# Performance work log

Hardware: AMD Instinct MI355X
Metric: run time of the kernel (lower is better)

## Reference

```python
import jax, jax.numpy as jnp
import numpy as np

B, L, D, H = 2, 2048, 768, 12
DH = D // H          # 64
DFF = 4 * D          # 3072
ALPHA = 0.25         # lorentz_alpha
BLEND = 0.5          # blend for FFN and MinkowskiLayerNorm (set via set_blend)
EPS = 1e-5
SCALE = float(np.sqrt(DH))


def setup_inputs() -> dict:
    key = jax.random.key(0)
    ks = jax.random.split(key, 14)
    w = lambda k, shape: jax.random.normal(k, shape, jnp.float32) * 0.02
    causal = jnp.tril(jnp.ones((L, L), bool))
    attention_mask = jnp.where(causal, 0.0, -1e9).astype(jnp.float32)[None, None]
    return {
        'x': jax.random.normal(ks[0], (B, L, D), jnp.float32),
        'attention_mask': attention_mask,
        'timelike_mask': jax.random.bernoulli(ks[1], 0.25, (D,)),
        'Wq': w(ks[2], (D, D)), 'Wk': w(ks[3], (D, D)),
        'Wv': w(ks[4], (D, D)), 'Wo': w(ks[5], (D, D)),
        'w1': w(ks[6], (DFF, D)), 'w2': w(ks[7], (D, DFF)),
        'w1_t': w(ks[8], (DFF // 2, D)), 'w2_t': w(ks[9], (D, DFF // 2)),
        'w1_s': w(ks[10], (DFF // 2, D)), 'w2_s': w(ks[11], (D, DFF // 2)),
        'n1_w': jnp.ones(D, jnp.float32), 'n1_b': jnp.zeros(D, jnp.float32),
        'n2_w': jnp.ones(D, jnp.float32), 'n2_b': jnp.zeros(D, jnp.float32),
    }


def _mink_norm(x, m, w, b):
    # Minkowski LayerNorm blended with standard LN (m: float timelike mask)
    mean = x.mean(-1, keepdims=True)
    xc = x - mean
    var = (xc * xc).mean(-1, keepdims=True)
    x_std = xc / jnp.sqrt(var + EPS)
    sq = xc * xc
    eta = (sq * (1.0 - m)).sum(-1, keepdims=True) - (sq * m).sum(-1, keepdims=True)
    x_eta = xc / jnp.sqrt(jnp.abs(eta) + EPS)
    xn = (1.0 - BLEND) * x_std + BLEND * x_eta
    return w * xn + b


def _attn(x, attention_mask, m, Wq, Wk, Wv, Wo):
    # (B,L,D) -> (B,H,L,DH)
    split = lambda t: t.reshape(B, L, H, DH).transpose(0, 2, 1, 3)
    Q = split(x @ Wq.T)
    K = split(x @ Wk.T)
    V = split(x @ Wv.T)
    scores = jnp.einsum('bhqd,bhkd->bhqk', Q, K) / SCALE
    # Minkowski timelike correction: per-head diagonal mask on Q
    m2 = m.reshape(H, DH)[None, :, None, :]          # (1,H,1,DH)
    Q_t = Q * m2
    q_norm = jnp.linalg.norm(Q, axis=-1, keepdims=True)
    qt_norm = jnp.linalg.norm(Q_t, axis=-1, keepdims=True)
    sf = jnp.where(qt_norm > 1e-6, q_norm / jnp.maximum(qt_norm, 1e-8), 0.0)
    time_inner = jnp.einsum('bhqd,bhkd->bhqk', Q_t * sf, K) / SCALE
    scores = scores - 2.0 * ALPHA * time_inner
    scores = scores + attention_mask
    aw = jax.nn.softmax(scores, axis=-1)
    out = jnp.einsum('bhqk,bhkd->bhqd', aw, V)
    out = out.transpose(0, 2, 1, 3).reshape(B, L, D)
    return out @ Wo.T


def _ffn(x, m, w1, w2, w1_t, w2_t, w1_s, w2_s):
    std_out = jax.nn.gelu(x @ w1.T, approximate=False) @ w2.T
    h_t = jax.nn.silu((x * m) @ w1_t.T) @ w2_t.T
    h_s = jax.nn.gelu((x * (1.0 - m)) @ w1_s.T, approximate=False) @ w2_s.T
    return (1.0 - BLEND) * std_out + BLEND * (h_t + h_s)


def reference(x, attention_mask, timelike_mask, Wq, Wk, Wv, Wo,
              w1, w2, w1_t, w2_t, w1_s, w2_s, n1_w, n1_b, n2_w, n2_b):
    m = timelike_mask.astype(jnp.float32)
    ao = _attn(_mink_norm(x, m, n1_w, n1_b), attention_mask, m, Wq, Wk, Wv, Wo)
    x = x + ao
    x = x + _ffn(_mink_norm(x, m, n2_w, n2_b), m, w1, w2, w1_t, w2_t, w1_s, w2_s)
    return x
```

## Files before the change

### kernel.cpp

```cpp
#include <hip/hip_runtime.h>


typedef unsigned short u16;
typedef __bf16 bfrag __attribute__((ext_vector_type(8)));
typedef float f32x4 __attribute__((ext_vector_type(4)));

#define MFMA(a, b, c) __builtin_amdgcn_mfma_f32_16x16x32_bf16(a, b, c, 0, 0, 0)
#define NEG_BIG (-30000.0f)
#define ASYNC16(g, l)                                                        \
  __builtin_amdgcn_global_load_lds(                                          \
      (const __attribute__((address_space(1))) unsigned int*)(g),            \
      (__attribute__((address_space(3))) unsigned int*)(l), 16, 0, 0)

__device__ __forceinline__ float bf2f(u16 u) {
  unsigned int v = ((unsigned int)u) << 16;
  float f; __builtin_memcpy(&f, &v, 4); return f;
}
__device__ __forceinline__ u16 f2bf(float f) {
  unsigned int v; __builtin_memcpy(&v, &f, 4);
  v += 0x7fffu + ((v >> 16) & 1u);
  return (u16)(v >> 16);
}
__device__ __forceinline__ bfrag ldfrag(const u16* p) {
  bfrag v; __builtin_memcpy(&v, p, 16); return v;
}

__device__ __forceinline__ int xcd_work_id() {
  const int nx = gridDim.x, ny = gridDim.y;
  const int nwg = nx * ny * gridDim.z;
  const int orig = blockIdx.x + nx * (blockIdx.y + ny * blockIdx.z);
  if (nwg & 7) return orig;
  return (orig & 7) * (nwg >> 3) + (orig >> 3);
}

__global__ __launch_bounds__(256) void mask_conv_k(const void* __restrict__ mask,
                                                   float* __restrict__ mfl) {
  __shared__ int msh;
  if (threadIdx.x == 0) msh = 0;
  __syncthreads();
  const unsigned int* w = (const unsigned int*)mask;
  if (threadIdx.x < 192) {
    const unsigned int v = w[threadIdx.x];
    if ((v & 0xFFFFu) == 0x3F80u) atomicOr(&msh, 4);
    else if (v == 0x3F800000u) atomicOr(&msh, 2);
    else if (v >= 2u) atomicOr(&msh, 1);
  }
  __syncthreads();
  const int m = msh;
  const int mode = (m & 4) ? 3 : (m & 2) ? 2 : (m & 1) ? 1 : 0;
  for (int i = threadIdx.x; i < 768; i += 256) {
    int b;
    if (mode == 3) b = ((const u16*)mask)[i] != 0;
    else if (mode == 2) b = ((const float*)mask)[i] != 0.0f;
    else if (mode == 1) b = ((const unsigned char*)mask)[i] != 0;
    else b = ((const int*)mask)[i] != 0;
    mfl[i] = (float)b;
  }
}

struct Segs {
  const void* src[14];
  int off[14];
  int n[14];
  int mmode[14];
};

__global__ __launch_bounds__(256) void convert_k(Segs segs, u16* __restrict__ dstb,
                                                 const float* __restrict__ mfl) {
  const int seg = blockIdx.y;
  const int n = segs.n[seg];
  const int mm = segs.mmode[seg];
  u16* dst = dstb + segs.off[seg];
  const float* src = (const float*)segs.src[seg];
  for (int i = (blockIdx.x * 256 + threadIdx.x) * 4; i < n; i += gridDim.x * 1024) {
    float4 v;
    __builtin_memcpy(&v, src + i, 16);
    if (mm) {
      const int k = i % 768;
      float m0 = mfl[k], m1 = mfl[k + 1], m2 = mfl[k + 2], m3 = mfl[k + 3];
      if (mm == 2) { m0 = 1.f - m0; m1 = 1.f - m1; m2 = 1.f - m2; m3 = 1.f - m3; }
      v.x *= m0; v.y *= m1; v.z *= m2; v.w *= m3;
    }
    dst[i] = f2bf(v.x); dst[i + 1] = f2bf(v.y);
    dst[i + 2] = f2bf(v.z); dst[i + 3] = f2bf(v.w);
  }
}

__global__ __launch_bounds__(256) void mink_norm_k(
    const float* __restrict__ X, const float* __restrict__ mf,
    const u16* __restrict__ w, const u16* __restrict__ bias,
    u16* __restrict__ Y, float* __restrict__ Xcopy) {
  __shared__ float red[8];
  const int row = blockIdx.x, tid = threadIdx.x;
  const int wid = tid >> 6, lane = tid & 63;
  const size_t roff = (size_t)row * 768;

  float xv[3], mv[3];
  int idx[3];
#pragma unroll
  for (int i = 0; i < 3; i++) {
    idx[i] = tid + i * 256;
    xv[i] = X[roff + idx[i]];
    mv[i] = mf[idx[i]];
  }
  if (Xcopy) {
#pragma unroll
    for (int i = 0; i < 3; i++) Xcopy[roff + idx[i]] = xv[i];
  }
  float s = xv[0] + xv[1] + xv[2];
#pragma unroll
  for (int o = 32; o >= 1; o >>= 1) s += __shfl_xor(s, o, 64);
  if (lane == 0) red[wid] = s;
  __syncthreads();
  const float mean = (red[0] + red[1] + red[2] + red[3]) * (1.0f / 768.0f);
  __syncthreads();

  float xc[3], ss = 0.0f, sm = 0.0f;
#pragma unroll
  for (int i = 0; i < 3; i++) {
    xc[i] = xv[i] - mean;
    ss += xc[i] * xc[i];
    sm += xc[i] * xc[i] * mv[i];
  }
#pragma unroll
  for (int o = 32; o >= 1; o >>= 1) {
    ss += __shfl_xor(ss, o, 64);
    sm += __shfl_xor(sm, o, 64);
  }
  if (lane == 0) { red[wid] = ss; red[4 + wid] = sm; }
  __syncthreads();
  const float sumsq = red[0] + red[1] + red[2] + red[3];
  const float summ = red[4] + red[5] + red[6] + red[7];
  const float var = sumsq * (1.0f / 768.0f);
  const float eta = sumsq - 2.0f * summ;
  const float rs = 1.0f / sqrtf(var + 1e-5f);
  const float re = 1.0f / sqrtf(fabsf(eta) + 1e-5f);

#pragma unroll
  for (int i = 0; i < 3; i++) {
    const float xn = xc[i] * 0.5f * (rs + re);
    Y[roff + idx[i]] = f2bf(bf2f(w[idx[i]]) * xn + bf2f(bias[idx[i]]));
  }
}

__global__ __launch_bounds__(256) void qcorr_k(u16* __restrict__ Q,
                                               const float* __restrict__ mf) {
  const int idx = blockIdx.x * 4 + (threadIdx.x >> 6);
  const int t = threadIdx.x & 63;
  const int h = idx % 12;
  const int bl = idx / 12;
  const size_t off = (size_t)bl * 768 + h * 64 + t;
  const float q = bf2f(Q[off]);
  const float m = mf[h * 64 + t];
  float q2 = q * q, qm2 = q * q * m;
#pragma unroll
  for (int o = 32; o >= 1; o >>= 1) {
    q2 += __shfl_xor(q2, o, 64);
    qm2 += __shfl_xor(qm2, o, 64);
  }
  const float qn = sqrtf(q2), qtn = sqrtf(qm2);
  const float sf = (qtn > 1e-6f) ? qn / fmaxf(qtn, 1e-8f) : 0.0f;
  Q[off] = f2bf(q * (1.0f - 0.5f * sf * m) * 0.125f);
}

__device__ __forceinline__ void gemm128_loop(
    const u16* __restrict__ Ab, const u16* __restrict__ Wb2,
    int K, int lda, int ldb, u16 (*As)[32], u16 (*Bs)[32], f32x4 acc[4][4]) {
  const int tid = threadIdx.x;
  const int wid = tid >> 6, lane = tid & 63;
  const int lr = lane & 15, lq = lane >> 4;
  const int srow = wid * 32 + (lane >> 2);
  const int scol = (lane & 3) * 8;
  const u16* ga0 = Ab + (size_t)srow * lda + scol;
  const u16* ga1 = Ab + (size_t)(srow + 16) * lda + scol;
  const u16* gb0 = Wb2 + (size_t)srow * ldb + scol;
  const u16* gb1 = Wb2 + (size_t)(srow + 16) * ldb + scol;
  const int wr = (wid >> 1) * 64, wc = (wid & 1) * 64;
  const int nt = K >> 5;

#define STAGE16(dbuf, k0)                                                    \
  {                                                                          \
    u16* _a0 = &As[(dbuf) * 128 + wid * 32][0];                              \
    u16* _a1 = &As[(dbuf) * 128 + wid * 32 + 16][0];                         \
    u16* _b0 = &Bs[(dbuf) * 128 + wid * 32][0];                              \
    u16* _b1 = &Bs[(dbuf) * 128 + wid * 32 + 16][0];                         \
    ASYNC16(ga0 + (k0), _a0);                                                \
    ASYNC16(ga1 + (k0), _a1);                                                \
    ASYNC16(gb0 + (k0), _b0);                                                \
    ASYNC16(gb1 + (k0), _b1);                                                \
  }

  STAGE16(0, 0);
  for (int t = 0; t < nt; ++t) {
    const int cur = t & 1;
    if (t + 1 < nt) {
      STAGE16(cur ^ 1, (t + 1) << 5);
      __builtin_amdgcn_sched_barrier(0);
      asm volatile("s_waitcnt vmcnt(4)" ::: "memory");
    } else {
      asm volatile("s_waitcnt vmcnt(0)" ::: "memory");
    }
    __builtin_amdgcn_s_barrier();
    __builtin_amdgcn_sched_barrier(0);
    bfrag af[4], bf4[4];
#pragma unroll
    for (int i = 0; i < 4; i++)
      af[i] = ldfrag(&As[cur * 128 + wr + i * 16 + lr][lq * 8]);
#pragma unroll
    for (int j = 0; j < 4; j++)
      bf4[j] = ldfrag(&Bs[cur * 128 + wc + j * 16 + lr][lq * 8]);
#pragma unroll
    for (int i = 0; i < 4; i++)
#pragma unroll
      for (int j = 0; j < 4; j++)
        acc[i][j] = MFMA(af[i], bf4[j], acc[i][j]);
    asm volatile("s_waitcnt lgkmcnt(0)" ::: "memory");
    __builtin_amdgcn_sched_barrier(0);
    __builtin_amdgcn_s_barrier();
  }
#undef STAGE16
}

__device__ __forceinline__ void gemm128x64_loop(
    const u16* __restrict__ Ab, const u16* __restrict__ Wb2,
    int K, int lda, int ldb, u16 (*As)[32], u16 (*Bs)[32], f32x4 acc[4][2]) {
  const int tid = threadIdx.x;
  const int wid = tid >> 6, lane = tid & 63;
  const int lr = lane & 15, lq = lane >> 4;
  const int srowA = wid * 32 + (lane >> 2);
  const int srowB = wid * 16 + (lane >> 2);
  const int scol = (lane & 3) * 8;
  const u16* ga0 = Ab + (size_t)srowA * lda + scol;
  const u16* ga1 = Ab + (size_t)(srowA + 16) * lda + scol;
  const u16* gb0 = Wb2 + (size_t)srowB * ldb + scol;
  const int wr = (wid >> 1) * 64, wc = (wid & 1) * 32;
  const int nt = K >> 5;

#define STAGE64(dbuf, k0)                                                    \
  {                                                                          \
    u16* _a0 = &As[(dbuf) * 128 + wid * 32][0];                              \
    u16* _a1 = &As[(dbuf) * 128 + wid * 32 + 16][0];                         \
    u16* _b0 = &Bs[(dbuf) * 64 + wid * 16][0];                               \
    ASYNC16(ga0 + (k0), _a0);                                                \
    ASYNC16(ga1 + (k0), _a1);                                                \
    ASYNC16(gb0 + (k0), _b0);                                                \
  }

  STAGE64(0, 0);
  for (int t = 0; t < nt; ++t) {
    const int cur = t & 1;
    if (t + 1 < nt) {
      STAGE64(cur ^ 1, (t + 1) << 5);
      __builtin_amdgcn_sched_barrier(0);
      asm volatile("s_waitcnt vmcnt(3)" ::: "memory");
    } else {
      asm volatile("s_waitcnt vmcnt(0)" ::: "memory");
    }
    __builtin_amdgcn_s_barrier();
    __builtin_amdgcn_sched_barrier(0);
    bfrag af[4], bf2[2];
#pragma unroll
    for (int i = 0; i < 4; i++)
      af[i] = ldfrag(&As[cur * 128 + wr + i * 16 + lr][lq * 8]);
#pragma unroll
    for (int j = 0; j < 2; j++)
      bf2[j] = ldfrag(&Bs[cur * 64 + wc + j * 16 + lr][lq * 8]);
#pragma unroll
    for (int i = 0; i < 4; i++)
#pragma unroll
      for (int j = 0; j < 2; j++)
        acc[i][j] = MFMA(af[i], bf2[j], acc[i][j]);
    asm volatile("s_waitcnt lgkmcnt(0)" ::: "memory");
    __builtin_amdgcn_sched_barrier(0);
    __builtin_amdgcn_s_barrier();
  }
#undef STAGE64
}

struct GSeg { const u16* W; u16* C; int ldc; int nblk; int epi; };
struct GArgs { GSeg s[3]; };

__global__ __launch_bounds__(256) void gemm128_fused(
    const u16* __restrict__ A, int lda, int K, GArgs args) {
  __shared__ __align__(16) u16 As[256][32];
  __shared__ __align__(16) u16 Bs[256][32];
  const int w = xcd_work_id();
  int cb = w % gridDim.x, seg = 0;
  const int by = w / gridDim.x;
  while (cb >= args.s[seg].nblk) { cb -= args.s[seg].nblk; seg++; }
  const GSeg g = args.s[seg];
  const int rowb = by * 128, colb = cb * 128;
  f32x4 acc[4][4] = {};
  gemm128_loop(A + (size_t)rowb * lda, g.W + (size_t)colb * K, K, lda, K,
               As, Bs, acc);

  const int lane = threadIdx.x & 63, wid = threadIdx.x >> 6;
  const int lr = lane & 15, lq = lane >> 4;
  const int wr = (wid >> 1) * 64, wc = (wid & 1) * 64;
#pragma unroll
  for (int i = 0; i < 4; i++)
#pragma unroll
    for (int j = 0; j < 4; j++)
#pragma unroll
      for (int r = 0; r < 4; r++) {
        const int row = rowb + wr + i * 16 + lq * 4 + r;
        const int col = colb + wc + j * 16 + lr;
        float v = acc[i][j][r];
        if (g.epi == 2) v = 0.5f * v * (1.0f + erff(v * 0.70710678118654752f));
        else if (g.epi == 3) v = v / (1.0f + __expf(-v));
        g.C[(size_t)row * g.ldc + col] = f2bf(v);
      }
}

__global__ __launch_bounds__(256) void gemm128_wo_splitk(
    const u16* __restrict__ A, const u16* __restrict__ W,
    float* __restrict__ Out) {
  __shared__ __align__(16) u16 As[256][32];
  __shared__ __align__(16) u16 Bs[256][32];
  const int w = xcd_work_id();
  const int bx = w % gridDim.x;
  const int by = (w / gridDim.x) % gridDim.y;
  const int z = w / (gridDim.x * gridDim.y);
  const int rowb = by * 128, colb = bx * 128;
  f32x4 acc[4][4] = {};
  gemm128_loop(A + (size_t)rowb * 768 + z * 384,
               W + (size_t)colb * 768 + z * 384, 384, 768, 768, As, Bs, acc);

  const int lane = threadIdx.x & 63, wid = threadIdx.x >> 6;
  const int lr = lane & 15, lq = lane >> 4;
  const int wr = (wid >> 1) * 64, wc = (wid & 1) * 64;
#pragma unroll
  for (int i = 0; i < 4; i++)
#pragma unroll
    for (int j = 0; j < 4; j++)
#pragma unroll
      for (int r = 0; r < 4; r++) {
        const int row = rowb + wr + i * 16 + lq * 4 + r;
        const int col = colb + wc + j * 16 + lr;
        atomicAdd(&Out[(size_t)row * 768 + col], acc[i][j][r]);
      }
}

__global__ __launch_bounds__(256) void ffn2_splitk64(
    const u16* __restrict__ H1, const u16* __restrict__ Ht,
    const u16* __restrict__ Hs, const u16* __restrict__ W2,
    const u16* __restrict__ W2t, const u16* __restrict__ W2s,
    float* __restrict__ Out) {
  __shared__ __align__(16) u16 As[256][32];
  __shared__ __align__(16) u16 Bs[128][32];
  const int w = xcd_work_id();
  const int bx = w % gridDim.x;
  const int by = (w / gridDim.x) % gridDim.y;
  const int z = w / (gridDim.x * gridDim.y);
  const int rowb = by * 128, colb = bx * 64;
  f32x4 acc[4][2] = {};
  if (z == 0)
    gemm128x64_loop(H1 + (size_t)rowb * 3072, W2 + (size_t)colb * 3072,
                    1536, 3072, 3072, As, Bs, acc);
  else if (z == 1)
    gemm128x64_loop(H1 + (size_t)rowb * 3072 + 1536,
                    W2 + (size_t)colb * 3072 + 1536,
                    1536, 3072, 3072, As, Bs, acc);
  else if (z == 2)
    gemm128x64_loop(Ht + (size_t)rowb * 1536, W2t + (size_t)colb * 1536,
                    1536, 1536, 1536, As, Bs, acc);
  else
    gemm128x64_loop(Hs + (size_t)rowb * 1536, W2s + (size_t)colb * 1536,
                    1536, 1536, 1536, As, Bs, acc);

  const int lane = threadIdx.x & 63, wid = threadIdx.x >> 6;
  const int lr = lane & 15, lq = lane >> 4;
  const int wr = (wid >> 1) * 64, wc = (wid & 1) * 32;
#pragma unroll
  for (int i = 0; i < 4; i++)
#pragma unroll
    for (int j = 0; j < 2; j++)
#pragma unroll
      for (int r = 0; r < 4; r++) {
        const int row = rowb + wr + i * 16 + lq * 4 + r;
        const int col = colb + wc + j * 16 + lr;
        atomicAdd(&Out[(size_t)row * 768 + col], 0.5f * acc[i][j][r]);
      }
}

__global__ __launch_bounds__(256) void flash_attn_k(
    const u16* __restrict__ Qc, const u16* __restrict__ Kb,
    const u16* __restrict__ Vb, u16* __restrict__ O,
    float* __restrict__ Pn, float* __restrict__ Ph) {
  __shared__ __align__(16) u16 Ks[64][40];
  __shared__ __align__(16) u16 Vt[64][72];
  __shared__ __align__(16) u16 Ps[4][16][72];
  const int tid = threadIdx.x, wid = tid >> 6, lane = tid & 63;
  const int lr = lane & 15, lq = lane >> 4;

  int bx = blockIdx.x, qt = 0, c = 0;
  for (int q = 31; q >= 0; --q) {
    const int nc = (q < 8) ? 1 : (q / 8 + 1);
    if (bx < nc) { qt = q; c = bx; break; }
    bx -= nc;
  }
  const int nt = qt + 1;
  const int t0 = c * 8;
  const int t1 = (t0 + 8 < nt) ? t0 + 8 : nt;

  const int qb = qt * 64;
  const int bh = blockIdx.y;
  const int b = bh / 12, h = bh % 12;
  const int q0 = qb + wid * 16;
  const size_t base = (size_t)b * 2048 * 768 + h * 64;

  bfrag aq[2];
  aq[0] = ldfrag(Qc + base + (size_t)(q0 + lr) * 768 + lq * 8);
  aq[1] = ldfrag(Qc + base + (size_t)(q0 + lr) * 768 + 32 + lq * 8);

  f32x4 o[4] = {};
  float mrow[4] = {NEG_BIG, NEG_BIG, NEG_BIG, NEG_BIG};
  float lrow[4] = {0.0f, 0.0f, 0.0f, 0.0f};

  const int krow = tid >> 3;
  const int kcol = (tid & 7) * 8;
  const int vkey = tid & 31;
  const int vdg = tid >> 5;

  const u16* kp = Kb + base + (size_t)(t0 * 64 + krow) * 768 + kcol;
  const u16* vp = Vb + base + (size_t)(t0 * 64 + vkey) * 768 + vdg * 8;

  uint4 kv0, kv1, vv0, vv1;
  __builtin_memcpy(&kv0, kp, 16);
  __builtin_memcpy(&kv1, kp + (size_t)32 * 768, 16);
  __builtin_memcpy(&vv0, vp, 16);
  __builtin_memcpy(&vv1, vp + (size_t)32 * 768, 16);

  for (int kt = t0; kt < t1; kt++) {
    __syncthreads();
    __builtin_memcpy(&Ks[krow][kcol], &kv0, 16);
    __builtin_memcpy(&Ks[krow + 32][kcol], &kv1, 16);
    {
      union { uint4 u; u16 s[8]; } a, b2;
      a.u = vv0; b2.u = vv1;
#pragma unroll
      for (int j = 0; j < 8; j++) {
        Vt[vdg * 8 + j][vkey] = a.s[j];
        Vt[vdg * 8 + j][vkey + 32] = b2.s[j];
      }
    }
    __syncthreads();
    if (kt + 1 < t1) {
      const size_t koff = (size_t)(kt + 1 - t0) * 64 * 768;
      __builtin_memcpy(&kv0, kp + koff, 16);
      __builtin_memcpy(&kv1, kp + koff + (size_t)32 * 768, 16);
      __builtin_memcpy(&vv0, vp + koff, 16);
      __builtin_memcpy(&vv1, vp + koff + (size_t)32 * 768, 16);
    }

    const int kbk = kt * 64;
    {
      f32x4 s4[4] = {};
#pragma unroll
      for (int kg = 0; kg < 2; kg++) {
#pragma unroll
        for (int cc = 0; cc < 4; cc++) {
          bfrag bk = ldfrag(&Ks[cc * 16 + lr][kg * 32 + lq * 8]);
          s4[cc] = MFMA(aq[kg], bk, s4[cc]);
        }
      }
#pragma unroll
      for (int r = 0; r < 4; r++) {
        const int q = q0 + lq * 4 + r;
        float v[4];
        float mx = NEG_BIG;
#pragma unroll
        for (int cc = 0; cc < 4; cc++) {
          v[cc] = (kbk + cc * 16 + lr > q) ? NEG_BIG : s4[cc][r];
          mx = fmaxf(mx, v[cc]);
        }
#pragma unroll
        for (int off = 8; off >= 1; off >>= 1)
          mx = fmaxf(mx, __shfl_xor(mx, off, 16));
        const float mn = fmaxf(mrow[r], mx);
        const float alpha = __expf(mrow[r] - mn);
        float sm = 0.0f;
        float p[4];
#pragma unroll
        for (int cc = 0; cc < 4; cc++) {
          p[cc] = __expf(v[cc] - mn);
          sm += p[cc];
        }
#pragma unroll
        for (int off = 8; off >= 1; off >>= 1) sm += __shfl_xor(sm, off, 16);
        lrow[r] = lrow[r] * alpha + sm;
        mrow[r] = mn;
#pragma unroll
        for (int dt = 0; dt < 4; dt++) o[dt][r] *= alpha;
#pragma unroll
        for (int cc = 0; cc < 4; cc++)
          Ps[wid][lq * 4 + r][cc * 16 + lr] = f2bf(p[cc]);
      }
      __threadfence_block();
      bfrag pf0 = ldfrag(&Ps[wid][lr][lq * 8]);
      bfrag pf1 = ldfrag(&Ps[wid][lr][32 + lq * 8]);
#pragma unroll
      for (int dt = 0; dt < 4; dt++) {
        bfrag v0 = ldfrag(&Vt[dt * 16 + lr][lq * 8]);
        bfrag v1 = ldfrag(&Vt[dt * 16 + lr][32 + lq * 8]);
        o[dt] = MFMA(pf0, v0, o[dt]);
        o[dt] = MFMA(pf1, v1, o[dt]);
      }
    }
  }

  if (qt < 8) {
#pragma unroll
    for (int r = 0; r < 4; r++) {
      const float inv = 1.0f / fmaxf(lrow[r], 1e-30f);
      const int q = q0 + lq * 4 + r;
#pragma unroll
      for (int dt = 0; dt < 4; dt++)
        O[base + (size_t)q * 768 + dt * 16 + lr] = f2bf(o[dt][r] * inv);
    }
  } else {
    int off = 0;
    for (int j = 8; j < qt; ++j) off += j / 8 + 1;
    const int s = bh * 72 + off + c;
    float* Op = (s < 1536) ? Pn + (size_t)s * 4096
                           : Ph + (size_t)(s - 1536) * 4096;
    float* lmp = Ph + 786432 + (size_t)s * 128;
#pragma unroll
    for (int r = 0; r < 4; r++) {
      const int row = wid * 16 + lq * 4 + r;
#pragma unroll
      for (int dt = 0; dt < 4; dt++)
        Op[(size_t)row * 64 + dt * 16 + lr] = o[dt][r];
      if (lr == 0) { lmp[row] = mrow[r]; lmp[64 + row] = lrow[r]; }
    }
  }
}

__global__ __launch_bounds__(256) void attn_merge_k(
    const float* __restrict__ Pn, const float* __restrict__ Ph,
    u16* __restrict__ O) {
  const int qt = 8 + blockIdx.x;
  const int bh = blockIdx.y;
  const int b = bh / 12, h = bh % 12;
  const int nc = qt / 8 + 1;
  int off = 0;
  for (int j = 8; j < qt; ++j) off += j / 8 + 1;
  const int s0 = bh * 72 + off;
  const int row = threadIdx.x >> 2;
  const int c0 = (threadIdx.x & 3) * 16;
  const float* lmb = Ph + 786432;

  float mg = NEG_BIG;
  for (int cc = 0; cc < nc; ++cc)
    mg = fmaxf(mg, lmb[(size_t)(s0 + cc) * 128 + row]);

  float acc[16];
#pragma unroll
  for (int j = 0; j < 16; j++) acc[j] = 0.0f;
  float lg = 0.0f;
  for (int cc = 0; cc < nc; ++cc) {
    const int s = s0 + cc;
    const float mcv = lmb[(size_t)s * 128 + row];
    const float coef = __expf(mcv - mg);
    lg += coef * lmb[(size_t)s * 128 + 64 + row];
    const float* Op = (s < 1536) ? Pn + (size_t)s * 4096
                                 : Ph + (size_t)(s - 1536) * 4096;
    const float* rp = Op + (size_t)row * 64 + c0;
#pragma unroll
    for (int g = 0; g < 4; g++) {
      float4 v;
      __builtin_memcpy(&v, rp + g * 4, 16);
      acc[g * 4 + 0] += coef * v.x;
      acc[g * 4 + 1] += coef * v.y;
      acc[g * 4 + 2] += coef * v.z;
      acc[g * 4 + 3] += coef * v.w;
    }
  }
  const float inv = 1.0f / fmaxf(lg, 1e-30f);
  const int q = qt * 64 + row;
  const size_t ob = (size_t)b * 2048 * 768 + h * 64 + (size_t)q * 768 + c0;
#pragma unroll
  for (int j = 0; j < 16; j++) O[ob + j] = f2bf(acc[j] * inv);
}

extern "C" void kernel_launch(void* const* d_in, const int* in_sizes, int n_in,
                              void* d_out, int out_size, void* d_ws,
                              size_t ws_size, hipStream_t stream) {
  (void)in_sizes; (void)n_in; (void)out_size; (void)ws_size;
  const float* x = (const float*)d_in[0];
  const void* mask = d_in[2];

  char* ws = (char*)d_ws;
  u16* Wb  = (u16*)(ws);
  u16* n1h = (u16*)(ws + 23599104);
  u16* Qb  = (u16*)(ws + 48764928);
  u16* Kb2 = (u16*)(ws + 55056384);
  u16* Vb2 = (u16*)(ws + 61347840);
  u16* att = (u16*)(ws + 67639296);
  u16* hs  = (u16*)(ws + 80222208);
  float* mfl = (float*)(ws + 92805120);
  float* x1 = (float*)d_out;
  float* Pn = (float*)n1h;
  float* Ph = (float*)hs;

  u16* Wq = Wb + 0,        *Wk = Wb + 589824,   *Wv = Wb + 1179648;
  u16* Wo = Wb + 1769472,  *w1 = Wb + 2359296,  *w1t = Wb + 4718592;
  u16* w1s = Wb + 5898240, *w2 = Wb + 7077888,  *w2t = Wb + 9437184;
  u16* w2s = Wb + 10616832;
  u16* n1w = Wb + 11796480, *n1b = Wb + 11797248;
  u16* n2w = Wb + 11798016, *n2b = Wb + 11798784;

  Segs sg;
  const int srcidx[14] = {3, 4, 5, 6, 7, 9, 11, 8, 10, 12, 13, 14, 15, 16};
  const int offs[14] = {0, 589824, 1179648, 1769472, 2359296, 4718592,
                        5898240, 7077888, 9437184, 10616832,
                        11796480, 11797248, 11798016, 11798784};
  const int ns[14] = {589824, 589824, 589824, 589824, 2359296, 1179648,
                      1179648, 2359296, 1179648, 1179648, 768, 768, 768, 768};
  const int mms[14] = {0, 0, 0, 0, 0, 1, 2, 0, 0, 0, 0, 0, 0, 0};
  for (int i = 0; i < 14; i++) {
    sg.src[i] = d_in[srcidx[i]];
    sg.off[i] = offs[i];
    sg.n[i] = ns[i];
    sg.mmode[i] = mms[i];
  }

  mask_conv_k<<<1, 256, 0, stream>>>(mask, mfl);
  convert_k<<<dim3(2304, 14), 256, 0, stream>>>(sg, Wb, mfl);

  mink_norm_k<<<4096, 256, 0, stream>>>(x, mfl, n1w, n1b, n1h, x1);

  GArgs qkv;
  qkv.s[0] = {Wq, Qb, 768, 6, 0};
  qkv.s[1] = {Wk, Kb2, 768, 6, 0};
  qkv.s[2] = {Wv, Vb2, 768, 6, 0};
  gemm128_fused<<<dim3(18, 32), 256, 0, stream>>>(n1h, 768, 768, qkv);

  qcorr_k<<<12288, 256, 0, stream>>>(Qb, mfl);

  flash_attn_k<<<dim3(80, 24), 256, 0, stream>>>(Qb, Kb2, Vb2, att, Pn, Ph);
  attn_merge_k<<<dim3(24, 24), 256, 0, stream>>>(Pn, Ph, att);

  gemm128_wo_splitk<<<dim3(6, 32, 2), 256, 0, stream>>>(att, Wo, x1);

  mink_norm_k<<<4096, 256, 0, stream>>>(x1, mfl, n2w, n2b, Qb, nullptr);

  GArgs ffn1;
  ffn1.s[0] = {w1, n1h, 3072, 24, 2};
  ffn1.s[1] = {w1t, att, 1536, 12, 3};
  ffn1.s[2] = {w1s, hs, 1536, 12, 2};
  gemm128_fused<<<dim3(48, 32), 256, 0, stream>>>(Qb, 768, 768, ffn1);

  ffn2_splitk64<<<dim3(12, 32, 4), 256, 0, stream>>>(n1h, att, hs, w2, w2t,
                                                     w2s, (float*)d_out);
}
```

Baseline: 434.2 us.

## Fuse Q timelike correction into QKV GEMM epilogue and swap GEMM tile shapes

The Q-norm timelike rescaling is moved into the QKV GEMM epilogue. Per-row norms over each 64-wide head are reduced with 16-lane shuffles across the accumulator tile, so the separate qcorr kernel and its extra read and write of Q are gone. The Wo split-K GEMM now uses 128x64 tiles, giving more blocks. The FFN2 split-K GEMM goes the other way, from 128x64 to 128x128 tiles, cutting the block count and the redundant A loads. The epilogue adds shuffle and register work, and the tile changes shift occupancy and atomic traffic.

New measurement: 421.5 us. 1.03x faster.

```diff
diff --git a/kernel.cpp b/kernel.cpp
--- a/kernel.cpp
+++ b/kernel.cpp
@@ -143,26 +143,6 @@
   }
 }
 
-__global__ __launch_bounds__(256) void qcorr_k(u16* __restrict__ Q,
-                                               const float* __restrict__ mf) {
-  const int idx = blockIdx.x * 4 + (threadIdx.x >> 6);
-  const int t = threadIdx.x & 63;
-  const int h = idx % 12;
-  const int bl = idx / 12;
-  const size_t off = (size_t)bl * 768 + h * 64 + t;
-  const float q = bf2f(Q[off]);
-  const float m = mf[h * 64 + t];
-  float q2 = q * q, qm2 = q * q * m;
-#pragma unroll
-  for (int o = 32; o >= 1; o >>= 1) {
-    q2 += __shfl_xor(q2, o, 64);
-    qm2 += __shfl_xor(qm2, o, 64);
-  }
-  const float qn = sqrtf(q2), qtn = sqrtf(qm2);
-  const float sf = (qtn > 1e-6f) ? qn / fmaxf(qtn, 1e-8f) : 0.0f;
-  Q[off] = f2bf(q * (1.0f - 0.5f * sf * m) * 0.125f);
-}
-
 __device__ __forceinline__ void gemm128_loop(
     const u16* __restrict__ Ab, const u16* __restrict__ Wb2,
     int K, int lda, int ldb, u16 (*As)[32], u16 (*Bs)[32], f32x4 acc[4][4]) {
@@ -281,7 +261,8 @@
 struct GArgs { GSeg s[3]; };
 
 __global__ __launch_bounds__(256) void gemm128_fused(
-    const u16* __restrict__ A, int lda, int K, GArgs args) {
+    const u16* __restrict__ A, int lda, int K, GArgs args,
+    const float* __restrict__ mfl) {
   __shared__ __align__(16) u16 As[256][32];
   __shared__ __align__(16) u16 Bs[256][32];
   const int w = xcd_work_id();
@@ -297,6 +278,41 @@
   const int lane = threadIdx.x & 63, wid = threadIdx.x >> 6;
   const int lr = lane & 15, lq = lane >> 4;
   const int wr = (wid >> 1) * 64, wc = (wid & 1) * 64;
+
+  if (g.epi == 1) {
+    const int cb64 = colb + wc;
+    float mj[4];
+#pragma unroll
+    for (int j = 0; j < 4; j++) mj[j] = mfl[cb64 + j * 16 + lr];
+#pragma unroll
+    for (int i = 0; i < 4; i++)
+#pragma unroll
+      for (int r = 0; r < 4; r++) {
+        float p2 = 0.0f, pm2 = 0.0f;
+#pragma unroll
+        for (int j = 0; j < 4; j++) {
+          const float v = acc[i][j][r];
+          p2 += v * v;
+          pm2 += v * v * mj[j];
+        }
+#pragma unroll
+        for (int off = 8; off >= 1; off >>= 1) {
+          p2 += __shfl_xor(p2, off, 64);
+          pm2 += __shfl_xor(pm2, off, 64);
+        }
+        const float qn = sqrtf(p2), qtn = sqrtf(pm2);
+        const float sf = (qtn > 1e-6f) ? qn / fmaxf(qtn, 1e-8f) : 0.0f;
+        const int row = rowb + wr + i * 16 + lq * 4 + r;
+#pragma unroll
+        for (int j = 0; j < 4; j++) {
+          const int col = cb64 + j * 16 + lr;
+          const float v = acc[i][j][r] * (1.0f - 0.5f * sf * mj[j]) * 0.125f;
+          g.C[(size_t)row * g.ldc + col] = f2bf(v);
+        }
+      }
+    return;
+  }
+
 #pragma unroll
   for (int i = 0; i < 4; i++)
 #pragma unroll
@@ -314,6 +330,38 @@
 
 __global__ __launch_bounds__(256) void gemm128_wo_splitk(
     const u16* __restrict__ A, const u16* __restrict__ W,
+    float* __restrict__ Out) {
+  __shared__ __align__(16) u16 As[256][32];
+  __shared__ __align__(16) u16 Bs[128][32];
+  const int w = xcd_work_id();
+  const int bx = w % gridDim.x;
+  const int by = (w / gridDim.x) % gridDim.y;
+  const int z = w / (gridDim.x * gridDim.y);
+  const int rowb = by * 128, colb = bx * 64;
+  f32x4 acc[4][2] = {};
+  gemm128x64_loop(A + (size_t)rowb * 768 + z * 384,
+                  W + (size_t)colb * 768 + z * 384, 384, 768, 768,
+                  As, Bs, acc);
+
+  const int lane = threadIdx.x & 63, wid = threadIdx.x >> 6;
+  const int lr = lane & 15, lq = lane >> 4;
+  const int wr = (wid >> 1) * 64, wc = (wid & 1) * 32;
+#pragma unroll
+  for (int i = 0; i < 4; i++)
+#pragma unroll
+    for (int j = 0; j < 2; j++)
+#pragma unroll
+      for (int r = 0; r < 4; r++) {
+        const int row = rowb + wr + i * 16 + lq * 4 + r;
+        const int col = colb + wc + j * 16 + lr;
+        atomicAdd(&Out[(size_t)row * 768 + col], acc[i][j][r]);
+      }
+}
+
+__global__ __launch_bounds__(256) void ffn2_splitk(
+    const u16* __restrict__ H1, const u16* __restrict__ Ht,
+    const u16* __restrict__ Hs, const u16* __restrict__ W2,
+    const u16* __restrict__ W2t, const u16* __restrict__ W2s,
     float* __restrict__ Out) {
   __shared__ __align__(16) u16 As[256][32];
   __shared__ __align__(16) u16 Bs[256][32];
@@ -323,8 +371,19 @@
   const int z = w / (gridDim.x * gridDim.y);
   const int rowb = by * 128, colb = bx * 128;
   f32x4 acc[4][4] = {};
-  gemm128_loop(A + (size_t)rowb * 768 + z * 384,
-               W + (size_t)colb * 768 + z * 384, 384, 768, 768, As, Bs, acc);
+  if (z == 0)
+    gemm128_loop(H1 + (size_t)rowb * 3072, W2 + (size_t)colb * 3072,
+                 1536, 3072, 3072, As, Bs, acc);
+  else if (z == 1)
+    gemm128_loop(H1 + (size_t)rowb * 3072 + 1536,
+                 W2 + (size_t)colb * 3072 + 1536,
+                 1536, 3072, 3072, As, Bs, acc);
+  else if (z == 2)
+    gemm128_loop(Ht + (size_t)rowb * 1536, W2t + (size_t)colb * 1536,
+                 1536, 1536, 1536, As, Bs, acc);
+  else
+    gemm128_loop(Hs + (size_t)rowb * 1536, W2s + (size_t)colb * 1536,
+                 1536, 1536, 1536, As, Bs, acc);
 
   const int lane = threadIdx.x & 63, wid = threadIdx.x >> 6;
   const int lr = lane & 15, lq = lane >> 4;
@@ -333,48 +392,6 @@
   for (int i = 0; i < 4; i++)
 #pragma unroll
     for (int j = 0; j < 4; j++)
-#pragma unroll
-      for (int r = 0; r < 4; r++) {
-        const int row = rowb + wr + i * 16 + lq * 4 + r;
-        const int col = colb + wc + j * 16 + lr;
-        atomicAdd(&Out[(size_t)row * 768 + col], acc[i][j][r]);
-      }
-}
-
-__global__ __launch_bounds__(256) void ffn2_splitk64(
-    const u16* __restrict__ H1, const u16* __restrict__ Ht,
-    const u16* __restrict__ Hs, const u16* __restrict__ W2,
-    const u16* __restrict__ W2t, const u16* __restrict__ W2s,
-    float* __restrict__ Out) {
-  __shared__ __align__(16) u16 As[256][32];
-  __shared__ __align__(16) u16 Bs[128][32];
-  const int w = xcd_work_id();
-  const int bx = w % gridDim.x;
-  const int by = (w / gridDim.x) % gridDim.y;
-  const int z = w / (gridDim.x * gridDim.y);
-  const int rowb = by * 128, colb = bx * 64;
-  f32x4 acc[4][2] = {};
-  if (z == 0)
-    gemm128x64_loop(H1 + (size_t)rowb * 3072, W2 + (size_t)colb * 3072,
-                    1536, 3072, 3072, As, Bs, acc);
-  else if (z == 1)
-    gemm128x64_loop(H1 + (size_t)rowb * 3072 + 1536,
-                    W2 + (size_t)colb * 3072 + 1536,
-                    1536, 3072, 3072, As, Bs, acc);
-  else if (z == 2)
-    gemm128x64_loop(Ht + (size_t)rowb * 1536, W2t + (size_t)colb * 1536,
-                    1536, 1536, 1536, As, Bs, acc);
-  else
-    gemm128x64_loop(Hs + (size_t)rowb * 1536, W2s + (size_t)colb * 1536,
-                    1536, 1536, 1536, As, Bs, acc);
-
-  const int lane = threadIdx.x & 63, wid = threadIdx.x >> 6;
-  const int lr = lane & 15, lq = lane >> 4;
-  const int wr = (wid >> 1) * 64, wc = (wid & 1) * 32;
-#pragma unroll
-  for (int i = 0; i < 4; i++)
-#pragma unroll
-    for (int j = 0; j < 2; j++)
 #pragma unroll
       for (int r = 0; r < 4; r++) {
         const int row = rowb + wr + i * 16 + lq * 4 + r;
@@ -631,17 +648,15 @@
   mink_norm_k<<<4096, 256, 0, stream>>>(x, mfl, n1w, n1b, n1h, x1);
 
   GArgs qkv;
-  qkv.s[0] = {Wq, Qb, 768, 6, 0};
+  qkv.s[0] = {Wq, Qb, 768, 6, 1};
   qkv.s[1] = {Wk, Kb2, 768, 6, 0};
   qkv.s[2] = {Wv, Vb2, 768, 6, 0};
-  gemm128_fused<<<dim3(18, 32), 256, 0, stream>>>(n1h, 768, 768, qkv);
-
-  qcorr_k<<<12288, 256, 0, stream>>>(Qb, mfl);
+  gemm128_fused<<<dim3(18, 32), 256, 0, stream>>>(n1h, 768, 768, qkv, mfl);
 
   flash_attn_k<<<dim3(80, 24), 256, 0, stream>>>(Qb, Kb2, Vb2, att, Pn, Ph);
   attn_merge_k<<<dim3(24, 24), 256, 0, stream>>>(Pn, Ph, att);
 
-  gemm128_wo_splitk<<<dim3(6, 32, 2), 256, 0, stream>>>(att, Wo, x1);
+  gemm128_wo_splitk<<<dim3(12, 32, 2), 256, 0, stream>>>(att, Wo, x1);
 
   mink_norm_k<<<4096, 256, 0, stream>>>(x1, mfl, n2w, n2b, Qb, nullptr);
 
@@ -649,8 +664,8 @@
   ffn1.s[0] = {w1, n1h, 3072, 24, 2};
   ffn1.s[1] = {w1t, att, 1536, 12, 3};
   ffn1.s[2] = {w1s, hs, 1536, 12, 2};
-  gemm128_fused<<<dim3(48, 32), 256, 0, stream>>>(Qb, 768, 768, ffn1);
-
-  ffn2_splitk64<<<dim3(12, 32, 4), 256, 0, stream>>>(n1h, att, hs, w2, w2t,
-                                                     w2s, (float*)d_out);
-}
+  gemm128_fused<<<dim3(48, 32), 256, 0, stream>>>(Qb, 768, 768, ffn1, mfl);
+
+  ffn2_splitk<<<dim3(6, 32, 4), 256, 0, stream>>>(n1h, att, hs, w2, w2t, w2s,
+                                                  (float*)d_out);
+}
```
